# Performance work log

Measured on AMD Instinct MI355X. Metric: run time of the kernel, lower is better.

Reference implementation:

```python
import jax, jax.numpy as jnp
import numpy as np

B, N, C, O, R = 8, 1024, 768, 768, 16  # batch, tokens, in_features, out_features, rank


def setup_inputs() -> dict:
    key = jax.random.key(0)
    k1, k2, k3, k4 = jax.random.split(key, 4)
    x = jax.random.normal(k1, (B, N, C), dtype=jnp.float32)
    coef = jax.random.normal(k2, (N, R), dtype=jnp.float32)
    # params: weight (out_features, in_features, rank), bias (out_features, rank)
    weight = 0.02 * jax.random.normal(k3, (O, C, R), dtype=jnp.float32)
    bias = 0.02 * jax.random.normal(k4, (O, R), dtype=jnp.float32)
    return {"x": x, "coef": coef, "weight": weight, "bias": bias}


def reference(x, coef, weight, bias):
    # Original math: per-token weight W_n[o,c] = sum_r coef[n,r] * weight[o,c,r]
    #                out[b,n,o] = sum_c x[b,n,c] * W_n[o,c] + sum_r coef[n,r]*bias[o,r]
    # Fused form: contract in_features first, rank last; avoids the (N,O,C) tensor.
    t = jnp.einsum('bnc,ocr->bnor', x, weight)   # (B,N,O,R)
    out = jnp.einsum('bnor,nr->bno', t, coef)    # (B,N,O)
    out = out + coef @ bias.T                    # (N,O) broadcast over batch
    return out
```

## Files before the change

kernel.cpp:

```cpp
#include <hip/hip_runtime.h>

#define NN 1024
#define CC 768
#define OO 768
#define RR 16
#define MM 8192
#define KK (CC*RR)
#define BM 128
#define BO 128
#define BK 64
#define KTILES (KK/BK)
#define KHALF (KTILES/2)

typedef __bf16 bf16x8 __attribute__((ext_vector_type(8)));
typedef float  f32x4  __attribute__((ext_vector_type(4)));

__global__ __launch_bounds__(256) void k_prep(const float* __restrict__ w,
                                              const float* __restrict__ coef,
                                              const float* __restrict__ bias,
                                              __bf16* __restrict__ bfrag,
                                              float* __restrict__ bterm,
                                              float* __restrict__ outz) {
    long id = blockIdx.x;
    if (id < 4608) {
        long t = id * 256 + threadIdx.x;
        int lrow = (int)(t & 15);
        int quad = (int)((t >> 4) & 3);
        int ks   = (int)((t >> 6) & 1);
        int o16  = (int)((t >> 7) & 7);
        int rest = (int)(t >> 10);
        int kt = rest % 192, ot = rest / 192;
        int o = ot * 128 + o16 * 16 + lrow;
        int c = kt * 4 + ks * 2 + (quad >> 1);
        const float* src = w + ((long)o * CC + c) * RR + (quad & 1) * 8;
        float4 a = *(const float4*)src;
        float4 b = *(const float4*)(src + 4);
        bf16x8 v = {(__bf16)a.x, (__bf16)a.y, (__bf16)a.z, (__bf16)a.w,
                    (__bf16)b.x, (__bf16)b.y, (__bf16)b.z, (__bf16)b.w};
        *(bf16x8*)(bfrag + t * 8) = v;
    } else if (id < 7680) {
        int i = (int)(id - 4608) * 256 + threadIdx.x;
        int n = i / OO, o = i - n * OO;
        const float4* cp = (const float4*)(coef + n * RR);
        const float4* bp = (const float4*)(bias + o * RR);
        float s = 0.f;
#pragma unroll
        for (int q = 0; q < 4; ++q) {
            float4 c4 = cp[q], b4 = bp[q];
            s += c4.x * b4.x + c4.y * b4.y + c4.z * b4.z + c4.w * b4.w;
        }
        bterm[i] = s;
    } else {
        long u = ((id - 7680) * 256 + threadIdx.x) * 8;
        float4 z = {0.f, 0.f, 0.f, 0.f};
        *(float4*)(outz + u) = z;
        *(float4*)(outz + u + 4) = z;
    }
}

__global__ __launch_bounds__(256, 3) void k_gemm(const float* __restrict__ x,
                                                 const float* __restrict__ coef,
                                                 const __bf16* __restrict__ bfrag,
                                                 const float* __restrict__ bterm,
                                                 float* __restrict__ out) {
    __shared__ __bf16 lA[2][BM * BK];

    const int tid = threadIdx.x;

    int g     = (blockIdx.x & 7) * 96 + (blockIdx.x >> 3);
    int ot    = g >> 7;
    int rem   = g & 127;
    int kh    = rem & 1;
    int mtile = rem >> 1;
    const int m0 = mtile * BM;
    const int kt0 = kh * KHALF, kt1 = kt0 + KHALF;

    const int am     = tid & 127;
    const int ahalf  = tid >> 7;
    const int m_glob = m0 + am;
    const int n_idx  = m_glob & (NN - 1);
    const float* xrow = x + (long)m_glob * CC;

    float cf[16];
#pragma unroll
    for (int r = 0; r < 16; r += 4) {
        float4 t4 = *(const float4*)(coef + n_idx * RR + r);
        cf[r] = t4.x; cf[r + 1] = t4.y; cf[r + 2] = t4.z; cf[r + 3] = t4.w;
    }

    const int lane = tid & 63, wave = tid >> 6;
    const int wm = (wave & 1) * 64, wo = (wave >> 1) * 64;
    const int lrow = lane & 15, quad = lane >> 4;

    const __bf16* Bk = bfrag + ((long)ot * 192 + kt0) * 8192
                     + (wo >> 4) * 1024 + quad * 128 + lrow * 8;

    f32x4 acc[4][4] = {};
    float2 x2 = *(const float2*)(xrow + kt0 * 4 + 2 * ahalf);

#pragma unroll 1
    for (int kt = kt0; kt < kt1; ++kt) {
        bf16x8 bfr[2][4];
#pragma unroll
        for (int ks = 0; ks < 2; ++ks)
#pragma unroll
            for (int io = 0; io < 4; ++io)
                bfr[ks][io] = *(const bf16x8*)(Bk + io * 1024 + ks * 512);
        Bk += 8192;

        float2 x2n = x2;
        if (kt + 1 < kt1) x2n = *(const float2*)(xrow + (kt + 1) * 4 + 2 * ahalf);

        __bf16* la = &lA[kt & 1][0];
#pragma unroll
        for (int ci = 0; ci < 2; ++ci) {
            float xv = ci ? x2.y : x2.x;
            int c_local = 2 * ahalf + ci;
#pragma unroll
            for (int rh = 0; rh < 2; ++rh) {
                bf16x8 v;
#pragma unroll
                for (int j = 0; j < 8; ++j) v[j] = (__bf16)(xv * cf[rh * 8 + j]);
                int kb = c_local * 2 + rh;
                *(bf16x8*)(&la[am * BK + ((kb ^ (am & 7)) * 8)]) = v;
            }
        }
        x2 = x2n;
        __syncthreads();

#pragma unroll
        for (int ks = 0; ks < 2; ++ks) {
            bf16x8 af[4];
            int kb = ks * 4 + quad;
#pragma unroll
            for (int im = 0; im < 4; ++im) {
                int row = wm + im * 16 + lrow;
                af[im] = *(const bf16x8*)(&la[row * BK + ((kb ^ (row & 7)) * 8)]);
            }
#pragma unroll
            for (int im = 0; im < 4; ++im)
#pragma unroll
                for (int io = 0; io < 4; ++io)
                    acc[im][io] = __builtin_amdgcn_mfma_f32_16x16x32_bf16(
                        af[im], bfr[ks][io], acc[im][io], 0, 0, 0);
        }
    }

#pragma unroll
    for (int im = 0; im < 4; ++im) {
#pragma unroll
        for (int io = 0; io < 4; ++io) {
            int o = ot * BO + wo + io * 16 + lrow;
#pragma unroll
            for (int r = 0; r < 4; ++r) {
                int moff = wm + im * 16 + quad * 4 + r;
                long m = m0 + moff;
                int n = (int)(m & (NN - 1));
                float v = acc[im][io][r];
                if (kh == 0) v += bterm[(long)n * OO + o];
                atomicAdd(&out[m * OO + o], v);
            }
        }
    }
}

__global__ void k_naive(const float* __restrict__ x, const float* __restrict__ coef,
                        const float* __restrict__ w, const float* __restrict__ bias,
                        float* __restrict__ out) {
    long i = (long)blockIdx.x * 256 + threadIdx.x;
    if (i >= (long)MM * OO) return;
    int o = (int)(i % OO);
    long m = i / OO;
    int n = (int)(m & (NN - 1));
    float cf[16];
#pragma unroll
    for (int r = 0; r < 16; ++r) cf[r] = coef[n * RR + r];
    const float* xr = x + m * CC;
    const float* wr = w + (long)o * CC * RR;
    float s = 0.f;
    for (int c = 0; c < CC; ++c) {
        float t = 0.f;
#pragma unroll
        for (int r = 0; r < 16; ++r) t += cf[r] * wr[c * RR + r];
        s += xr[c] * t;
    }
    float bs = 0.f;
#pragma unroll
    for (int r = 0; r < 16; ++r) bs += cf[r] * bias[o * RR + r];
    out[i] = s + bs;
}

extern "C" void kernel_launch(void* const* d_in, const int* in_sizes, int n_in,
                              void* d_out, int out_size, void* d_ws, size_t ws_size,
                              hipStream_t stream) {
    const float* x    = (const float*)d_in[0];
    const float* coef = (const float*)d_in[1];
    const float* w    = (const float*)d_in[2];
    const float* bias = (const float*)d_in[3];
    float* out = (float*)d_out;

    const size_t bfrag_bytes = (size_t)OO * KK * sizeof(__bf16);
    const size_t bt_bytes    = (size_t)NN * OO * sizeof(float);

    if (ws_size >= bfrag_bytes + bt_bytes) {
        __bf16* bfrag = (__bf16*)d_ws;
        float*  btrm  = (float*)((char*)d_ws + bfrag_bytes);
        k_prep<<<10752, 256, 0, stream>>>(w, coef, bias, bfrag, btrm, out);
        k_gemm<<<768, 256, 0, stream>>>(x, coef, bfrag, btrm, out);
    } else {
        k_naive<<<(int)(((long)MM * OO + 255) / 256), 256, 0, stream>>>(x, coef, w, bias, out);
    }
}
```

Before: 285.3 us.

## Halve GEMM M-tile, raise occupancy, and stage weight repack through LDS

```diff
diff --git a/kernel.cpp b/kernel.cpp
--- a/kernel.cpp
+++ b/kernel.cpp
@@ -6,13 +6,14 @@
 #define RR 16
 #define MM 8192
 #define KK (CC*RR)
-#define BM 128
+#define BM 64
 #define BO 128
 #define BK 64
 #define KTILES (KK/BK)
 #define KHALF (KTILES/2)
 
 typedef __bf16 bf16x8 __attribute__((ext_vector_type(8)));
+typedef __bf16 bf16x4 __attribute__((ext_vector_type(4)));
 typedef float  f32x4  __attribute__((ext_vector_type(4)));
 
 __global__ __launch_bounds__(256) void k_prep(const float* __restrict__ w,
@@ -21,25 +22,34 @@
                                               __bf16* __restrict__ bfrag,
                                               float* __restrict__ bterm,
                                               float* __restrict__ outz) {
-    long id = blockIdx.x;
-    if (id < 4608) {
-        long t = id * 256 + threadIdx.x;
-        int lrow = (int)(t & 15);
-        int quad = (int)((t >> 4) & 3);
-        int ks   = (int)((t >> 6) & 1);
-        int o16  = (int)((t >> 7) & 7);
-        int rest = (int)(t >> 10);
-        int kt = rest % 192, ot = rest / 192;
-        int o = ot * 128 + o16 * 16 + lrow;
-        int c = kt * 4 + ks * 2 + (quad >> 1);
-        const float* src = w + ((long)o * CC + c) * RR + (quad & 1) * 8;
-        float4 a = *(const float4*)src;
-        float4 b = *(const float4*)(src + 4);
-        bf16x8 v = {(__bf16)a.x, (__bf16)a.y, (__bf16)a.z, (__bf16)a.w,
-                    (__bf16)b.x, (__bf16)b.y, (__bf16)b.z, (__bf16)b.w};
-        *(bf16x8*)(bfrag + t * 8) = v;
-    } else if (id < 7680) {
-        int i = (int)(id - 4608) * 256 + threadIdx.x;
+    int id = blockIdx.x;
+    int t  = threadIdx.x;
+    if (id < 1152) {
+        __shared__ __bf16 ls[128 * 72];
+        int ot = id / 192, kt = id - ot * 192;
+        const float* base = w + ((long)(ot * 128) * CC + kt * 4) * RR;
+#pragma unroll
+        for (int s = 0; s < 8; ++s) {
+            int f4  = s * 256 + t;
+            int o_l = f4 >> 4;
+            int cr4 = f4 & 15;
+            float4 v = *(const float4*)(base + (long)o_l * (CC * RR) + cr4 * 4);
+            bf16x4 b = {(__bf16)v.x, (__bf16)v.y, (__bf16)v.z, (__bf16)v.w};
+            *(bf16x4*)(&ls[o_l * 72 + cr4 * 4]) = b;
+        }
+        __syncthreads();
+        long dst = ((long)ot * 192 + kt) * 8192;
+#pragma unroll
+        for (int ci = 0; ci < 4; ++ci) {
+            int ch   = t * 4 + ci;
+            int lrow = ch & 15, quad = (ch >> 4) & 3, ks = (ch >> 6) & 1, o16 = ch >> 7;
+            int o_l  = o16 * 16 + lrow;
+            int cr   = (ks * 2 + (quad >> 1)) * 16 + (quad & 1) * 8;
+            bf16x8 v = *(const bf16x8*)(&ls[o_l * 72 + cr]);
+            *(bf16x8*)(bfrag + dst + ch * 8) = v;
+        }
+    } else if (id < 1152 + 3072) {
+        int i = (id - 1152) * 256 + t;
         int n = i / OO, o = i - n * OO;
         const float4* cp = (const float4*)(coef + n * RR);
         const float4* bp = (const float4*)(bias + o * RR);
@@ -51,14 +61,14 @@
         }
         bterm[i] = s;
     } else {
-        long u = ((id - 7680) * 256 + threadIdx.x) * 8;
+        long u = ((long)(id - 4224) * 256 + t) * 8;
         float4 z = {0.f, 0.f, 0.f, 0.f};
         *(float4*)(outz + u) = z;
         *(float4*)(outz + u + 4) = z;
     }
 }
 
-__global__ __launch_bounds__(256, 3) void k_gemm(const float* __restrict__ x,
+__global__ __launch_bounds__(256, 6) void k_gemm(const float* __restrict__ x,
                                                  const float* __restrict__ coef,
                                                  const __bf16* __restrict__ bfrag,
                                                  const float* __restrict__ bterm,
@@ -67,36 +77,39 @@
 
     const int tid = threadIdx.x;
 
-    int g     = (blockIdx.x & 7) * 96 + (blockIdx.x >> 3);
-    int ot    = g >> 7;
-    int rem   = g & 127;
-    int kh    = rem & 1;
-    int mtile = rem >> 1;
+    int xcd = blockIdx.x & 7;
+    int s   = blockIdx.x >> 3;
+    int ot  = s >> 5;
+    int kh  = (s >> 4) & 1;
+    int mtl = s & 15;
+    int mtile = xcd * 16 + mtl;
     const int m0 = mtile * BM;
     const int kt0 = kh * KHALF, kt1 = kt0 + KHALF;
 
-    const int am     = tid & 127;
-    const int ahalf  = tid >> 7;
-    const int m_glob = m0 + am;
-    const int n_idx  = m_glob & (NN - 1);
-    const float* xrow = x + (long)m_glob * CC;
-
-    float cf[16];
-#pragma unroll
-    for (int r = 0; r < 16; r += 4) {
-        float4 t4 = *(const float4*)(coef + n_idx * RR + r);
-        cf[r] = t4.x; cf[r + 1] = t4.y; cf[r + 2] = t4.z; cf[r + 3] = t4.w;
+    const int arow = tid & 63;
+    const int h    = (tid >> 6) & 1;
+    const int rh   = tid >> 7;
+    const int m_g  = m0 + arow;
+    const int n_i  = m_g & (NN - 1);
+    const float* xrow = x + (long)m_g * CC;
+
+    float cf[8];
+    {
+        float4 a = *(const float4*)(coef + n_i * RR + rh * 8);
+        float4 b = *(const float4*)(coef + n_i * RR + rh * 8 + 4);
+        cf[0] = a.x; cf[1] = a.y; cf[2] = a.z; cf[3] = a.w;
+        cf[4] = b.x; cf[5] = b.y; cf[6] = b.z; cf[7] = b.w;
     }
 
     const int lane = tid & 63, wave = tid >> 6;
-    const int wm = (wave & 1) * 64, wo = (wave >> 1) * 64;
+    const int wm = (wave & 1) * 32, wo = (wave >> 1) * 64;
     const int lrow = lane & 15, quad = lane >> 4;
 
     const __bf16* Bk = bfrag + ((long)ot * 192 + kt0) * 8192
                      + (wo >> 4) * 1024 + quad * 128 + lrow * 8;
 
-    f32x4 acc[4][4] = {};
-    float2 x2 = *(const float2*)(xrow + kt0 * 4 + 2 * ahalf);
+    f32x4 acc[2][4] = {};
+    float2 x2 = *(const float2*)(xrow + kt0 * 4 + 2 * h);
 
 #pragma unroll 1
     for (int kt = kt0; kt < kt1; ++kt) {
@@ -109,54 +122,50 @@
         Bk += 8192;
 
         float2 x2n = x2;
-        if (kt + 1 < kt1) x2n = *(const float2*)(xrow + (kt + 1) * 4 + 2 * ahalf);
+        if (kt + 1 < kt1) x2n = *(const float2*)(xrow + (kt + 1) * 4 + 2 * h);
 
         __bf16* la = &lA[kt & 1][0];
 #pragma unroll
         for (int ci = 0; ci < 2; ++ci) {
             float xv = ci ? x2.y : x2.x;
-            int c_local = 2 * ahalf + ci;
-#pragma unroll
-            for (int rh = 0; rh < 2; ++rh) {
-                bf16x8 v;
-#pragma unroll
-                for (int j = 0; j < 8; ++j) v[j] = (__bf16)(xv * cf[rh * 8 + j]);
-                int kb = c_local * 2 + rh;
-                *(bf16x8*)(&la[am * BK + ((kb ^ (am & 7)) * 8)]) = v;
-            }
+            bf16x8 v;
+#pragma unroll
+            for (int j = 0; j < 8; ++j) v[j] = (__bf16)(xv * cf[j]);
+            int kb = (2 * h + ci) * 2 + rh;
+            *(bf16x8*)(&la[arow * BK + ((kb ^ (arow & 7)) * 8)]) = v;
         }
         x2 = x2n;
         __syncthreads();
 
 #pragma unroll
         for (int ks = 0; ks < 2; ++ks) {
-            bf16x8 af[4];
+            bf16x8 af[2];
             int kb = ks * 4 + quad;
 #pragma unroll
-            for (int im = 0; im < 4; ++im) {
-                int row = wm + im * 16 + lrow;
-                af[im] = *(const bf16x8*)(&la[row * BK + ((kb ^ (row & 7)) * 8)]);
+            for (int f = 0; f < 2; ++f) {
+                int row = wm + f * 16 + lrow;
+                af[f] = *(const bf16x8*)(&la[row * BK + ((kb ^ (row & 7)) * 8)]);
             }
 #pragma unroll
-            for (int im = 0; im < 4; ++im)
+            for (int f = 0; f < 2; ++f)
 #pragma unroll
                 for (int io = 0; io < 4; ++io)
-                    acc[im][io] = __builtin_amdgcn_mfma_f32_16x16x32_bf16(
-                        af[im], bfr[ks][io], acc[im][io], 0, 0, 0);
-        }
-    }
-
-#pragma unroll
-    for (int im = 0; im < 4; ++im) {
+                    acc[f][io] = __builtin_amdgcn_mfma_f32_16x16x32_bf16(
+                        af[f], bfr[ks][io], acc[f][io], 0, 0, 0);
+        }
+    }
+
+#pragma unroll
+    for (int f = 0; f < 2; ++f) {
 #pragma unroll
         for (int io = 0; io < 4; ++io) {
-            int o = ot * BO + wo + io * 16 + lrow;
+            int o = ot * 128 + wo + io * 16 + lrow;
 #pragma unroll
             for (int r = 0; r < 4; ++r) {
-                int moff = wm + im * 16 + quad * 4 + r;
+                int moff = wm + f * 16 + quad * 4 + r;
                 long m = m0 + moff;
                 int n = (int)(m & (NN - 1));
-                float v = acc[im][io][r];
+                float v = acc[f][io][r];
                 if (kh == 0) v += bterm[(long)n * OO + o];
                 atomicAdd(&out[m * OO + o], v);
             }
@@ -205,8 +214,8 @@
     if (ws_size >= bfrag_bytes + bt_bytes) {
         __bf16* bfrag = (__bf16*)d_ws;
         float*  btrm  = (float*)((char*)d_ws + bfrag_bytes);
-        k_prep<<<10752, 256, 0, stream>>>(w, coef, bias, bfrag, btrm, out);
-        k_gemm<<<768, 256, 0, stream>>>(x, coef, bfrag, btrm, out);
+        k_prep<<<7296, 256, 0, stream>>>(w, coef, bias, bfrag, btrm, out);
+        k_gemm<<<1536, 256, 0, stream>>>(x, coef, bfrag, btrm, out);
     } else {
         k_naive<<<(int)(((long)MM * OO + 255) / 256), 256, 0, stream>>>(x, coef, w, bias, out);
     }
```

Measured after the change: 709.0 us. 149% more time.

## Retile GEMM to 96-wide output tiles and seed output with bias in prep

Applied to the files above, without the earlier changes.

```diff
diff --git a/kernel.cpp b/kernel.cpp
--- a/kernel.cpp
+++ b/kernel.cpp
@@ -7,39 +7,47 @@
 #define MM 8192
 #define KK (CC*RR)
 #define BM 128
-#define BO 128
+#define BO 96
 #define BK 64
 #define KTILES (KK/BK)
 #define KHALF (KTILES/2)
 
 typedef __bf16 bf16x8 __attribute__((ext_vector_type(8)));
+typedef __bf16 bf16x4 __attribute__((ext_vector_type(4)));
 typedef float  f32x4  __attribute__((ext_vector_type(4)));
 
 __global__ __launch_bounds__(256) void k_prep(const float* __restrict__ w,
                                               const float* __restrict__ coef,
                                               const float* __restrict__ bias,
                                               __bf16* __restrict__ bfrag,
-                                              float* __restrict__ bterm,
-                                              float* __restrict__ outz) {
-    long id = blockIdx.x;
-    if (id < 4608) {
-        long t = id * 256 + threadIdx.x;
-        int lrow = (int)(t & 15);
-        int quad = (int)((t >> 4) & 3);
-        int ks   = (int)((t >> 6) & 1);
-        int o16  = (int)((t >> 7) & 7);
-        int rest = (int)(t >> 10);
-        int kt = rest % 192, ot = rest / 192;
-        int o = ot * 128 + o16 * 16 + lrow;
-        int c = kt * 4 + ks * 2 + (quad >> 1);
-        const float* src = w + ((long)o * CC + c) * RR + (quad & 1) * 8;
-        float4 a = *(const float4*)src;
-        float4 b = *(const float4*)(src + 4);
-        bf16x8 v = {(__bf16)a.x, (__bf16)a.y, (__bf16)a.z, (__bf16)a.w,
-                    (__bf16)b.x, (__bf16)b.y, (__bf16)b.z, (__bf16)b.w};
-        *(bf16x8*)(bfrag + t * 8) = v;
-    } else if (id < 7680) {
-        int i = (int)(id - 4608) * 256 + threadIdx.x;
+                                              float* __restrict__ out) {
+    int id = blockIdx.x;
+    int t  = threadIdx.x;
+    if (id < 2304) {
+        __shared__ __bf16 ls[16 * 260];
+        int o16 = id / 48, ktg = id - (id / 48) * 48;
+#pragma unroll
+        for (int s = 0; s < 4; ++s) {
+            int idx = s * 256 + t;
+            int o_l = idx >> 6, pos = idx & 63;
+            float4 v = *(const float4*)(w + (long)(o16 * 16 + o_l) * KK
+                                          + ktg * 256 + pos * 4);
+            bf16x4 b = {(__bf16)v.x, (__bf16)v.y, (__bf16)v.z, (__bf16)v.w};
+            *(bf16x4*)(&ls[o_l * 260 + pos * 4]) = b;
+        }
+        __syncthreads();
+        long dst = (long)(o16 * 192 + ktg * 4) * 1024;
+#pragma unroll
+        for (int s = 0; s < 2; ++s) {
+            int u = s * 256 + t;
+            int kt_l = u >> 7, ch = u & 127;
+            int ks = ch >> 6, quad = (ch >> 4) & 3, lrow = ch & 15;
+            int cr = (kt_l * 4 + ks * 2 + (quad >> 1)) * 16 + (quad & 1) * 8;
+            bf16x8 v = *(const bf16x8*)(&ls[lrow * 260 + cr]);
+            *(bf16x8*)(bfrag + dst + (long)kt_l * 1024 + ch * 8) = v;
+        }
+    } else {
+        int i = (id - 2304) * 256 + t;
         int n = i / OO, o = i - n * OO;
         const float4* cp = (const float4*)(coef + n * RR);
         const float4* bp = (const float4*)(bias + o * RR);
@@ -49,29 +57,24 @@
             float4 c4 = cp[q], b4 = bp[q];
             s += c4.x * b4.x + c4.y * b4.y + c4.z * b4.z + c4.w * b4.w;
         }
-        bterm[i] = s;
-    } else {
-        long u = ((id - 7680) * 256 + threadIdx.x) * 8;
-        float4 z = {0.f, 0.f, 0.f, 0.f};
-        *(float4*)(outz + u) = z;
-        *(float4*)(outz + u + 4) = z;
-    }
-}
-
-__global__ __launch_bounds__(256, 3) void k_gemm(const float* __restrict__ x,
+#pragma unroll
+        for (int b = 0; b < 8; ++b)
+            out[(long)(b * NN + n) * OO + o] = s;
+    }
+}
+
+__global__ __launch_bounds__(256, 4) void k_gemm(const float* __restrict__ x,
                                                  const float* __restrict__ coef,
                                                  const __bf16* __restrict__ bfrag,
-                                                 const float* __restrict__ bterm,
                                                  float* __restrict__ out) {
     __shared__ __bf16 lA[2][BM * BK];
 
     const int tid = threadIdx.x;
 
-    int g     = (blockIdx.x & 7) * 96 + (blockIdx.x >> 3);
-    int ot    = g >> 7;
-    int rem   = g & 127;
-    int kh    = rem & 1;
-    int mtile = rem >> 1;
+    const int ot    = blockIdx.x & 7;
+    const int loc   = blockIdx.x >> 3;
+    const int kh    = loc & 1;
+    const int mtile = loc >> 1;
     const int m0 = mtile * BM;
     const int kt0 = kh * KHALF, kt1 = kt0 + KHALF;
 
@@ -89,24 +92,28 @@
     }
 
     const int lane = tid & 63, wave = tid >> 6;
-    const int wm = (wave & 1) * 64, wo = (wave >> 1) * 64;
+    const int wm = (wave & 1) * 64, woq = wave >> 1;
     const int lrow = lane & 15, quad = lane >> 4;
 
-    const __bf16* Bk = bfrag + ((long)ot * 192 + kt0) * 8192
-                     + (wo >> 4) * 1024 + quad * 128 + lrow * 8;
-
-    f32x4 acc[4][4] = {};
+    const __bf16* Bk[3];
+#pragma unroll
+    for (int io = 0; io < 3; ++io) {
+        int o16 = ot * 6 + woq * 3 + io;
+        Bk[io] = bfrag + ((long)o16 * 192 + kt0) * 1024 + quad * 128 + lrow * 8;
+    }
+
+    f32x4 acc[4][3] = {};
     float2 x2 = *(const float2*)(xrow + kt0 * 4 + 2 * ahalf);
 
 #pragma unroll 1
     for (int kt = kt0; kt < kt1; ++kt) {
-        bf16x8 bfr[2][4];
-#pragma unroll
-        for (int ks = 0; ks < 2; ++ks)
-#pragma unroll
-            for (int io = 0; io < 4; ++io)
-                bfr[ks][io] = *(const bf16x8*)(Bk + io * 1024 + ks * 512);
-        Bk += 8192;
+        bf16x8 bfr[2][3];
+#pragma unroll
+        for (int io = 0; io < 3; ++io) {
+            bfr[0][io] = *(const bf16x8*)(Bk[io]);
+            bfr[1][io] = *(const bf16x8*)(Bk[io] + 512);
+            Bk[io] += 1024;
+        }
 
         float2 x2n = x2;
         if (kt + 1 < kt1) x2n = *(const float2*)(xrow + (kt + 1) * 4 + 2 * ahalf);
@@ -140,7 +147,7 @@
 #pragma unroll
             for (int im = 0; im < 4; ++im)
 #pragma unroll
-                for (int io = 0; io < 4; ++io)
+                for (int io = 0; io < 3; ++io)
                     acc[im][io] = __builtin_amdgcn_mfma_f32_16x16x32_bf16(
                         af[im], bfr[ks][io], acc[im][io], 0, 0, 0);
         }
@@ -149,16 +156,13 @@
 #pragma unroll
     for (int im = 0; im < 4; ++im) {
 #pragma unroll
-        for (int io = 0; io < 4; ++io) {
-            int o = ot * BO + wo + io * 16 + lrow;
+        for (int io = 0; io < 3; ++io) {
+            int o = ot * BO + woq * 48 + io * 16 + lrow;
 #pragma unroll
             for (int r = 0; r < 4; ++r) {
                 int moff = wm + im * 16 + quad * 4 + r;
                 long m = m0 + moff;
-                int n = (int)(m & (NN - 1));
-                float v = acc[im][io][r];
-                if (kh == 0) v += bterm[(long)n * OO + o];
-                atomicAdd(&out[m * OO + o], v);
+                atomicAdd(&out[m * OO + o], acc[im][io][r]);
             }
         }
     }
@@ -200,13 +204,11 @@
     float* out = (float*)d_out;
 
     const size_t bfrag_bytes = (size_t)OO * KK * sizeof(__bf16);
-    const size_t bt_bytes    = (size_t)NN * OO * sizeof(float);
-
-    if (ws_size >= bfrag_bytes + bt_bytes) {
+
+    if (ws_size >= bfrag_bytes) {
         __bf16* bfrag = (__bf16*)d_ws;
-        float*  btrm  = (float*)((char*)d_ws + bfrag_bytes);
-        k_prep<<<10752, 256, 0, stream>>>(w, coef, bias, bfrag, btrm, out);
-        k_gemm<<<768, 256, 0, stream>>>(x, coef, bfrag, btrm, out);
+        k_prep<<<5376, 256, 0, stream>>>(w, coef, bias, bfrag, out);
+        k_gemm<<<1024, 256, 0, stream>>>(x, coef, bfrag, out);
     } else {
         k_naive<<<(int)(((long)MM * OO + 255) / 256), 256, 0, stream>>>(x, coef, w, bias, out);
     }
```

New measurement: 285.9 us. No clear change (+0.2%).
